# Kernel tuning notes

Hardware: AMD Instinct MI355X
Metric: run time of the kernel (lower is better)

Reference implementation:

```python
import jax, jax.numpy as jnp
import numpy as np


def setup_inputs() -> dict:
    key = jax.random.key(0)
    k1, k2, k3, k4, k5 = jax.random.split(key, 5)
    B, S, D, F, E = 4, 4096, 1024, 2048, 8
    top_k = 2
    num_tokens = B * S
    capacity = max(int(num_tokens / E * 1.25), 4)  # 2560
    scale = 0.02
    return {
        "x": jax.random.normal(k1, (B, S, D), dtype=jnp.float32),
        "gate_w": jax.random.normal(k2, (D, E), dtype=jnp.float32) * scale,
        "w_gate": jax.random.normal(k3, (E, D, F), dtype=jnp.float32) * scale,
        "w_up": jax.random.normal(k4, (E, D, F), dtype=jnp.float32) * scale,
        "w_down": jax.random.normal(k5, (E, F, D), dtype=jnp.float32) * scale,
        "num_experts": E,
        "top_k": top_k,
        "capacity": capacity,
    }


AUX_LOSS_WEIGHT = 0.01


def reference(x, gate_w, w_gate, w_up, w_down, num_experts, top_k, capacity):
    B, S, D = x.shape
    N = B * S
    x_flat = x.reshape(N, D)

    # ---- Router ----
    logits = x_flat @ gate_w                      # [N, E]
    probs = jax.nn.softmax(logits, axis=-1)
    weights, indices = jax.lax.top_k(probs, top_k)  # [N, K]
    weights = weights / jnp.sum(weights, axis=-1, keepdims=True)

    # ---- Capacity-based dispatch ----
    indices_flat = indices.reshape(-1)            # [N*K]
    x_rep = jnp.repeat(x_flat, top_k, axis=0)     # [N*K, D]
    expert_mask = jax.nn.one_hot(indices_flat, num_experts, dtype=jnp.int32)  # [N*K, E]
    token_priority = jnp.cumsum(expert_mask, axis=0) * expert_mask
    token_rank = jnp.sum(token_priority, axis=1)  # [N*K], 1-based rank within expert
    valid = (token_rank > 0) & (token_rank <= capacity)
    gather_idx = indices_flat * capacity + (token_rank - 1)  # [N*K]

    total_slots = num_experts * capacity
    # drop-mode scatter: invalid rows are sent out-of-bounds and dropped
    safe_idx = jnp.where(valid, gather_idx, total_slots)
    dispatched = jnp.zeros((total_slots, D), dtype=x.dtype)
    dispatched = dispatched.at[safe_idx].set(x_rep, mode="drop")
    dispatched = dispatched.reshape(num_experts, capacity, D)  # [E, C, D]

    # ---- Fused experts (grouped BMM, SwiGLU) ----
    gate = jnp.einsum("ecd,edf->ecf", dispatched, w_gate)
    up = jnp.einsum("ecd,edf->ecf", dispatched, w_up)
    hidden = jax.nn.silu(gate) * up
    expert_out = jnp.einsum("ecf,efd->ecd", hidden, w_down)
    expert_out_flat = expert_out.reshape(total_slots, D)

    # ---- Combine (row-aligned gather; dropped tokens contribute zero) ----
    gathered = expert_out_flat[jnp.clip(gather_idx, 0, total_slots - 1)]
    combined = jnp.where(valid[:, None], gathered, jnp.zeros((), dtype=x.dtype))
    combined = combined.reshape(N, top_k, D)
    output = jnp.sum(combined * weights[:, :, None], axis=1)  # [N, D]

    # ---- Aux load-balance loss ----
    mask = jax.nn.one_hot(indices, num_experts, dtype=jnp.float32).sum(axis=1)  # [N, E]
    f = mask.sum(axis=0) / (N * top_k + 1e-9)
    P = probs.mean(axis=0)
    aux_loss = num_experts * jnp.sum(f * P) * AUX_LOSS_WEIGHT

    return output.reshape(B, S, D), aux_loss
```

## Files before the change

### kernel.cpp

```cpp
#include <hip/hip_runtime.h>
#include <stdint.h>

#define N_TOK 16384
#define DIM   1024
#define NEXP  8
#define FF    2048
#define CAP   2560
#define NSLOT (NEXP*CAP)

using f32x4  = __attribute__((ext_vector_type(4))) float;
using bf16x8 = __attribute__((ext_vector_type(8))) short;

__device__ __forceinline__ unsigned short f2bf(float f){
  union { float f; unsigned u; } c; c.f = f;
  unsigned u = c.u + 0x7FFFu + ((c.u >> 16) & 1u);
  return (unsigned short)(u >> 16);
}
__device__ __forceinline__ float bf2f(unsigned short h){
  union { unsigned u; float f; } c; c.u = ((unsigned)h) << 16; return c.f;
}

__device__ __forceinline__ void gld16(const unsigned short* g, unsigned short* l){
  __builtin_amdgcn_global_load_lds((__attribute__((address_space(1))) void*)(void*)g,
                                   (__attribute__((address_space(3))) void*)l,
                                   16, 0, 0);
}

#define HBAR __builtin_amdgcn_s_barrier()
#define LG0  asm volatile("s_waitcnt lgkmcnt(0)" ::: "memory")

__global__ __launch_bounds__(256) void k_router(
    const float* __restrict__ x, const float* __restrict__ gate_w,
    int* __restrict__ topidx, float* __restrict__ topw,
    float* __restrict__ wavepart)
{
  __shared__ float gwT[NEXP][DIM];
  int tid = threadIdx.x;
  for (int i = tid; i < DIM*NEXP; i += 256) gwT[i & 7][i >> 3] = gate_w[i];
  __syncthreads();
  int wave = tid >> 6, lane = tid & 63;
  int t = blockIdx.x * 4 + wave;
  const float* xr = x + (size_t)t * DIM;
  double acc[NEXP];
  #pragma unroll
  for (int e = 0; e < NEXP; e++) acc[e] = 0.0;
  for (int j = 0; j < DIM/64; j++){
    double xv = (double)xr[lane + 64*j];
    #pragma unroll
    for (int e = 0; e < NEXP; e++) acc[e] += xv * (double)gwT[e][lane + 64*j];
  }
  #pragma unroll
  for (int off = 32; off >= 1; off >>= 1){
    #pragma unroll
    for (int e = 0; e < NEXP; e++) acc[e] += __shfl_xor(acc[e], off, 64);
  }
  if (lane == 0){
    double m = acc[0];
    #pragma unroll
    for (int e = 1; e < NEXP; e++) m = fmax(m, acc[e]);
    double p[NEXP], Z = 0.0;
    #pragma unroll
    for (int e = 0; e < NEXP; e++){ p[e] = exp(acc[e] - m); Z += p[e]; }
    double invZ = 1.0 / Z;
    #pragma unroll
    for (int e = 0; e < NEXP; e++) p[e] *= invZ;
    float4* wp = (float4*)(wavepart + (size_t)t*NEXP);
    wp[0] = make_float4((float)p[0], (float)p[1], (float)p[2], (float)p[3]);
    wp[1] = make_float4((float)p[4], (float)p[5], (float)p[6], (float)p[7]);
    int i0 = 0; double p0 = p[0];
    #pragma unroll
    for (int e = 1; e < NEXP; e++) if (p[e] > p0){ p0 = p[e]; i0 = e; }
    int i1 = (i0 == 0) ? 1 : 0; double p1 = p[i1];
    #pragma unroll
    for (int e = 0; e < NEXP; e++) if (e != i0 && p[e] > p1){ p1 = p[e]; i1 = e; }
    double s = p0 + p1;
    topidx[t*2+0] = i0; topidx[t*2+1] = i1;
    topw [t*2+0] = (float)(p0/s); topw[t*2+1] = (float)(p1/s);
  }
}

__global__ __launch_bounds__(1024) void k_scan_tcv(
    const int* __restrict__ topidx, const float* __restrict__ wavepart,
    int* __restrict__ slot_token, int* __restrict__ tok_slots,
    float* __restrict__ aux_out,
    const float* __restrict__ wg, const float* __restrict__ wu, const float* __restrict__ wd,
    unsigned short* __restrict__ B1, unsigned short* __restrict__ wdT,
    const float* __restrict__ x, unsigned short* __restrict__ xb)
{
  __shared__ uint8_t smem[32768];
  const int t = threadIdx.x;
  const int bidx = blockIdx.x;

  if (bidx == 0){
    int (*sc)[NEXP] = (int(*)[NEXP])smem;
    const int base_i = t * 32;
    int ids[32];
    #pragma unroll
    for (int j = 0; j < 32; j++) ids[j] = topidx[base_i + j];
    int b[NEXP];
    #pragma unroll
    for (int e = 0; e < NEXP; e++) b[e] = 0;
    #pragma unroll
    for (int j = 0; j < 32; j++){
      #pragma unroll
      for (int e = 0; e < NEXP; e++) if (ids[j] == e) b[e]++;
    }
    #pragma unroll
    for (int e = 0; e < NEXP; e++) sc[t][e] = b[e];
    __syncthreads();
    for (int off = 1; off < 1024; off <<= 1){
      int tmp[NEXP];
      #pragma unroll
      for (int e = 0; e < NEXP; e++) tmp[e] = (t >= off) ? sc[t-off][e] : 0;
      __syncthreads();
      #pragma unroll
      for (int e = 0; e < NEXP; e++) sc[t][e] += tmp[e];
      __syncthreads();
    }
    int myb[NEXP];
    #pragma unroll
    for (int e = 0; e < NEXP; e++) myb[e] = sc[t][e] - b[e];
    int cnt[NEXP];
    #pragma unroll
    for (int e = 0; e < NEXP; e++) cnt[e] = sc[1023][e];
    #pragma unroll
    for (int j = 0; j < 32; j++){
      int slot = -1;
      #pragma unroll
      for (int e = 0; e < NEXP; e++){
        if (ids[j] == e){
          int r = myb[e]; myb[e] = r + 1;
          if (r < CAP){
            slot = e*CAP + r;
            slot_token[slot] = (base_i + j) >> 1;
          }
        }
      }
      tok_slots[base_i + j] = slot;
    }
    for (int idx = t; idx < NSLOT; idx += 1024){
      int e2 = idx / CAP, r2 = idx - e2*CAP;
      if (r2 >= cnt[e2]) slot_token[idx] = -1;
    }
    __syncthreads();
    float pe[NEXP];
    #pragma unroll
    for (int e = 0; e < NEXP; e++) pe[e] = 0.f;
    for (int i = t; i < N_TOK; i += 1024){
      const float4* pr = (const float4*)(wavepart + (size_t)i*NEXP);
      float4 v0 = pr[0], v1 = pr[1];
      pe[0] += v0.x; pe[1] += v0.y; pe[2] += v0.z; pe[3] += v0.w;
      pe[4] += v1.x; pe[5] += v1.y; pe[6] += v1.z; pe[7] += v1.w;
    }
    #pragma unroll
    for (int off = 32; off >= 1; off >>= 1){
      #pragma unroll
      for (int e = 0; e < NEXP; e++) pe[e] += __shfl_xor(pe[e], off, 64);
    }
    __syncthreads();
    float* scf = (float*)smem;
    const int wv = t >> 6, ln = t & 63;
    if (ln == 0){
      #pragma unroll
      for (int e = 0; e < NEXP; e++) scf[wv*NEXP + e] = pe[e];
    }
    __syncthreads();
    if (t == 0){
      float aux = 0.f;
      #pragma unroll
      for (int e = 0; e < NEXP; e++){
        float P = 0.f;
        for (int w = 0; w < 16; w++) P += scf[w*NEXP + e];
        P /= (float)N_TOK;
        float f = (float)cnt[e] / ((float)(N_TOK*2) + 1e-9f);
        aux += f * P;
      }
      aux_out[0] = (float)NEXP * aux * 0.01f;
    }
  } else if (bidx <= 12288){
    float (*tt)[65] = (float(*)[65])smem;
    const int bid = bidx - 1;
    const int z = bid >> 9, rem = bid & 511;
    const int mode = z >> 3, e = z & 7;
    const float* in; unsigned short* out; int R, C, ct, rt;
    if (mode < 2){
      in  = (mode == 0 ? wg : wu) + (size_t)e * DIM * FF;
      out = B1 + (size_t)e * 2 * FF * DIM;
      R = DIM; C = FF; ct = rem & 31; rt = rem >> 5;
    } else {
      in  = wd + (size_t)e * FF * DIM;
      out = wdT + (size_t)e * DIM * FF;
      R = FF; C = DIM; ct = rem >> 5; rt = rem & 31;
    }
    const int c0 = ct * 64, r0 = rt * 64;
    {
      int row = t >> 4, c4 = t & 15;
      float4 v = *(const float4*)(in + (size_t)(r0 + row)*C + c0 + c4*4);
      tt[c4*4+0][row] = v.x; tt[c4*4+1][row] = v.y;
      tt[c4*4+2][row] = v.z; tt[c4*4+3][row] = v.w;
    }
    __syncthreads();
    {
      int cl = t >> 4;
      int rs = (t & 15) * 4;
      int c  = c0 + cl;
      int orow = (mode == 0) ? ((c>>4)*32 + (c&15))
               : (mode == 1) ? ((c>>4)*32 + 16 + (c&15))
               : c;
      unsigned long long pk = 0;
      #pragma unroll
      for (int j = 0; j < 4; j++) pk |= (unsigned long long)f2bf(tt[cl][rs+j]) << (16*j);
      *(unsigned long long*)(out + (size_t)orow*R + r0 + rs) = pk;
    }
  } else {
    const int gb = bidx - 12289;
    size_t base = ((size_t)gb*1024 + t)*4;
    float4 v = *(const float4*)(x + base);
    unsigned long long pk =
        (unsigned long long)f2bf(v.x)
      | ((unsigned long long)f2bf(v.y) << 16)
      | ((unsigned long long)f2bf(v.z) << 32)
      | ((unsigned long long)f2bf(v.w) << 48);
    *(unsigned long long*)(xb + base) = pk;
  }
}

#define FRD(R_, RR, KS) (*(const bf16x8*)((R_) + (RR)*64 + ((((KS)) ^ l7) << 3)))

#define STGH(TYPE, KT2) {                                                          \
    unsigned short* R_ = lds + ((((KT2)&1)*4 + (TYPE)))*8192;                      \
    if ((TYPE) < 2){                                                               \
      if (EPI == 1){                                                               \
        gld16(Axb + aoff[(TYPE)&1][0] + (KT2)*64, R_ + (wave*8)*64);               \
        gld16(Axb + aoff[(TYPE)&1][1] + (KT2)*64, R_ + (64 + wave*8)*64);          \
      } else {                                                                     \
        gld16(a00 + (size_t)(((TYPE)&1)*128 +  0)*LDG + (KT2)*64, R_ + (wave*8)*64);      \
        gld16(a00 + (size_t)(((TYPE)&1)*128 + 64)*LDG + (KT2)*64, R_ + (64 + wave*8)*64); \
      }                                                                            \
    } else {                                                                       \
      gld16(b00 + (size_t)(((TYPE)&1)*128 +  0)*LDG + (KT2)*64, R_ + (wave*8)*64);        \
      gld16(b00 + (size_t)(((TYPE)&1)*128 + 64)*LDG + (KT2)*64, R_ + (64 + wave*8)*64);   \
    } }

#define MM8(AM, AN, AV, BV)                                                        \
  _Pragma("unroll")                                                                \
  for (int f = 0; f < 4; f++)                                                      \
    _Pragma("unroll")                                                              \
    for (int n = 0; n < 2; n++)                                                    \
      _Pragma("unroll")                                                            \
      for (int kk = 0; kk < 2; kk++)                                               \
        acc[(AM)+f][(AN)+n] = __builtin_amdgcn_mfma_f32_16x16x32_bf16(             \
            AV[f*2+kk], BV[n*2+kk], acc[(AM)+f][(AN)+n], 0, 0, 0);

template<int KDIM, int LDG, int EPI>
__global__ __launch_bounds__(512, 2) void k_gemm8(
    const unsigned short* __restrict__ A,
    const unsigned short* __restrict__ B,
    unsigned short* __restrict__ Out0,
    unsigned short* __restrict__ Out1,
    const int* __restrict__ slot_token)
{
  constexpr int NT    = KDIM / 64;
  constexpr int BROWS = (EPI == 1) ? 2*FF : DIM;
  constexpr int LDO   = (EPI == 1) ? FF : DIM;
  __shared__ unsigned short lds[65536];
  const int id = blockIdx.x;
  const int e  = id & 7;
  int t  = id >> 3;
  int ks = 0;
  if (EPI == 2){ ks = t & 1; t >>= 1; }
  const int mt = t % 10, nt = t / 10;
  const int m0 = mt*256, n0 = nt*256;
  const unsigned short* Ab = A + ((size_t)e*CAP   + m0) * LDG + (size_t)ks*KDIM;
  const unsigned short* Bb = B + ((size_t)e*BROWS + n0) * LDG + (size_t)ks*KDIM;
  const int tid = threadIdx.x, wave = tid >> 6, lane = tid & 63;
  const int wr = wave >> 2, wc = wave & 3;
  const int g = lane >> 4, l15 = lane & 15, l7 = l15 & 7;
  const int srow = lane >> 3, sslot = lane & 7;
  const int kslot_src = sslot ^ srow;

  const unsigned short* Axb = A + (size_t)kslot_src*8;
  unsigned int aoff[2][2];
  const unsigned short* a00 = Ab + (size_t)(wave*8 + srow)*LDG + kslot_src*8;
  const unsigned short* b00 = Bb + (size_t)(wave*8 + srow)*LDG + kslot_src*8;
  if (EPI == 1){
    #pragma unroll
    for (int ah = 0; ah < 2; ah++)
      #pragma unroll
      for (int j = 0; j < 2; j++){
        int row = m0 + ah*128 + j*64 + wave*8 + srow;
        int tk = slot_token[e*CAP + row];
        aoff[ah][j] = (unsigned)((tk < 0 ? 0 : tk) * DIM);
      }
  }

  f32x4 acc[8][4];
  const f32x4 z4 = {0.f,0.f,0.f,0.f};
  #pragma unroll
  for (int i = 0; i < 8; i++)
    #pragma unroll
    for (int n = 0; n < 4; n++) acc[i][n] = z4;

  STGH(0,0); STGH(1,0); STGH(2,0); STGH(3,0);
  STGH(0,1); STGH(1,1); STGH(2,1);
  asm volatile("s_waitcnt vmcnt(6)" ::: "memory");
  HBAR;

  for (int kt = 0; kt < NT; ++kt){
    const int b0 = (kt & 1)*4;
    unsigned short* RA = lds + (b0 + wr)*8192;
    unsigned short* RB = lds + (b0 + 2 + (wc >> 1))*8192;
    const int nb = (wc & 1)*64;
    bf16x8 a0[8], a1[8], bv[4], b2[4];

    #pragma unroll
    for (int f = 0; f < 4; f++)
      #pragma unroll
      for (int kk = 0; kk < 2; kk++)
        a0[f*2+kk] = FRD(RA, f*16 + l15, kk*4 + g);
    #pragma unroll
    for (int n = 0; n < 2; n++)
      #pragma unroll
      for (int kk = 0; kk < 2; kk++)
        bv[n*2+kk] = FRD(RB, nb + n*16 + l15, kk*4 + g);
    if (kt + 1 < NT) STGH(3, kt+1);
    HBAR; LG0;
    __builtin_amdgcn_s_setprio(1);  MM8(0, 0, a0, bv);  __builtin_amdgcn_s_setprio(0);

    #pragma unroll
    for (int f = 0; f < 4; f++)
      #pragma unroll
      for (int kk = 0; kk < 2; kk++)
        a1[f*2+kk] = FRD(RA, 64 + f*16 + l15, kk*4 + g);
    if (kt + 2 < NT) STGH(0, kt+2);
    HBAR; LG0;
    __builtin_amdgcn_s_setprio(1);  MM8(4, 0, a1, bv);  __builtin_amdgcn_s_setprio(0);

    #pragma unroll
    for (int n = 0; n < 2; n++)
      #pragma unroll
      for (int kk = 0; kk < 2; kk++)
        b2[n*2+kk] = FRD(RB, nb + 32 + n*16 + l15, kk*4 + g);
    if (kt + 2 < NT) STGH(1, kt+2);
    HBAR; LG0;
    __builtin_amdgcn_s_setprio(1);  MM8(4, 2, a1, b2);  __builtin_amdgcn_s_setprio(0);

    if (kt + 2 < NT) STGH(2, kt+2);
    __builtin_amdgcn_s_setprio(1);  MM8(0, 2, a0, b2);  __builtin_amdgcn_s_setprio(0);
    if (kt <= NT-3)      { asm volatile("s_waitcnt vmcnt(6)" ::: "memory"); }
    else if (kt == NT-2) { asm volatile("s_waitcnt vmcnt(0)" ::: "memory"); }
    HBAR;
  }

  if (EPI == 1){
    unsigned short* H = Out0 + ((size_t)e*CAP + m0 + wr*128) * (size_t)LDO;
    const int hc0 = (n0 + wc*64) >> 1;
    #pragma unroll
    for (int mf = 0; mf < 8; mf++)
      #pragma unroll
      for (int q = 0; q < 4; q++){
        int r = mf*16 + g*4 + q;
        #pragma unroll
        for (int p = 0; p < 2; p++){
          float gg = acc[mf][2*p][q], uu = acc[mf][2*p+1][q];
          float h = gg / (1.f + __expf(-gg)) * uu;
          H[(size_t)r*LDO + hc0 + p*16 + l15] = f2bf(h);
        }
      }
  } else {
    unsigned short* P = (ks ? Out1 : Out0);
    unsigned short* O = P + ((size_t)e*CAP + m0 + wr*128) * (size_t)LDO + n0 + wc*64;
    #pragma unroll
    for (int mf = 0; mf < 8; mf++)
      #pragma unroll
      for (int q = 0; q < 4; q++){
        int r = mf*16 + g*4 + q;
        #pragma unroll
        for (int n = 0; n < 4; n++)
          O[(size_t)r*LDO + n*16 + l15] = f2bf(acc[mf][n][q]);
      }
  }
}

__global__ __launch_bounds__(256) void k_combine(
    const unsigned short* __restrict__ P0, const unsigned short* __restrict__ P1,
    const int* __restrict__ tok_slots, const float* __restrict__ topw,
    float* __restrict__ out)
{
  const int t = blockIdx.x*2 + (threadIdx.x >> 7);
  const int tid = threadIdx.x & 127;
  const int s0 = tok_slots[t*2+0], s1 = tok_slots[t*2+1];
  const float w0 = topw[t*2+0], w1 = topw[t*2+1];
  float r[8];
  #pragma unroll
  for (int j = 0; j < 8; j++) r[j] = 0.f;
  if (s0 >= 0){
    bf16x8 v0 = *(const bf16x8*)(P0 + (size_t)s0*DIM + tid*8);
    bf16x8 v1 = *(const bf16x8*)(P1 + (size_t)s0*DIM + tid*8);
    #pragma unroll
    for (int j = 0; j < 8; j++)
      r[j] += w0 * (bf2f((unsigned short)v0[j]) + bf2f((unsigned short)v1[j]));
  }
  if (s1 >= 0){
    bf16x8 v0 = *(const bf16x8*)(P0 + (size_t)s1*DIM + tid*8);
    bf16x8 v1 = *(const bf16x8*)(P1 + (size_t)s1*DIM + tid*8);
    #pragma unroll
    for (int j = 0; j < 8; j++)
      r[j] += w1 * (bf2f((unsigned short)v0[j]) + bf2f((unsigned short)v1[j]));
  }
  float4* o = (float4*)(out + (size_t)t*DIM + tid*8);
  o[0] = make_float4(r[0], r[1], r[2], r[3]);
  o[1] = make_float4(r[4], r[5], r[6], r[7]);
}

extern "C" void kernel_launch(void* const* d_in, const int* in_sizes, int n_in,
                              void* d_out, int out_size, void* d_ws, size_t ws_size,
                              hipStream_t stream)
{
  const float* x      = (const float*)d_in[0];
  const float* gate_w = (const float*)d_in[1];
  const float* w_gate = (const float*)d_in[2];
  const float* w_up   = (const float*)d_in[3];
  const float* w_down = (const float*)d_in[4];
  float* out = (float*)d_out;

  uint8_t* ws = (uint8_t*)d_ws;
  int*   topidx       = (int*)ws;               ws += (size_t)N_TOK*2*4;
  float* topw         = (float*)ws;             ws += (size_t)N_TOK*2*4;
  int*   slot_token   = (int*)ws;               ws += (size_t)NSLOT*4;
  int*   tok_slots    = (int*)ws;               ws += (size_t)N_TOK*2*4;
  float* wavepart     = (float*)ws;             ws += (size_t)N_TOK*NEXP*4;
  unsigned short* xb     = (unsigned short*)ws; ws += (size_t)N_TOK*DIM*2;
  unsigned short* P0     = (unsigned short*)ws; ws += (size_t)NSLOT*DIM*2;
  unsigned short* hidden = (unsigned short*)ws; ws += (size_t)NSLOT*FF*2;
  unsigned short* B1     = (unsigned short*)ws; ws += (size_t)NEXP*2*FF*DIM*2;
  unsigned short* wdT    = (unsigned short*)ws; ws += (size_t)NEXP*DIM*FF*2;
  size_t need = (size_t)(ws - (uint8_t*)d_ws);
  if (ws_size < need) return;
  unsigned short* P1 = B1;

  k_router<<<N_TOK/4, 256, 0, stream>>>(x, gate_w, topidx, topw, wavepart);
  k_scan_tcv<<<16385, 1024, 0, stream>>>(topidx, wavepart, slot_token, tok_slots,
                                         out + (size_t)N_TOK*DIM,
                                         w_gate, w_up, w_down, B1, wdT, x, xb);
  k_gemm8<DIM, DIM, 1><<<1280, 512, 0, stream>>>(xb, B1, hidden, nullptr, slot_token);
  k_gemm8<DIM, FF, 2><<<640, 512, 0, stream>>>(hidden, wdT, P0, P1, nullptr);
  k_combine<<<N_TOK/2, 256, 0, stream>>>(P0, P1, tok_slots, topw, out);
}
```

Measured before the change: 423.3 us.

## Split 256x256 GEMM tile across 16 waves instead of 8

After: 560.1 us. 32.3% more time.

```diff
diff --git a/kernel.cpp b/kernel.cpp
--- a/kernel.cpp
+++ b/kernel.cpp
@@ -225,35 +225,14 @@
   }
 }
 
-#define FRD(R_, RR, KS) (*(const bf16x8*)((R_) + (RR)*64 + ((((KS)) ^ l7) << 3)))
-
-#define STGH(TYPE, KT2) {                                                          \
-    unsigned short* R_ = lds + ((((KT2)&1)*4 + (TYPE)))*8192;                      \
-    if ((TYPE) < 2){                                                               \
-      if (EPI == 1){                                                               \
-        gld16(Axb + aoff[(TYPE)&1][0] + (KT2)*64, R_ + (wave*8)*64);               \
-        gld16(Axb + aoff[(TYPE)&1][1] + (KT2)*64, R_ + (64 + wave*8)*64);          \
-      } else {                                                                     \
-        gld16(a00 + (size_t)(((TYPE)&1)*128 +  0)*LDG + (KT2)*64, R_ + (wave*8)*64);      \
-        gld16(a00 + (size_t)(((TYPE)&1)*128 + 64)*LDG + (KT2)*64, R_ + (64 + wave*8)*64); \
-      }                                                                            \
-    } else {                                                                       \
-      gld16(b00 + (size_t)(((TYPE)&1)*128 +  0)*LDG + (KT2)*64, R_ + (wave*8)*64);        \
-      gld16(b00 + (size_t)(((TYPE)&1)*128 + 64)*LDG + (KT2)*64, R_ + (64 + wave*8)*64);   \
-    } }
-
-#define MM8(AM, AN, AV, BV)                                                        \
-  _Pragma("unroll")                                                                \
-  for (int f = 0; f < 4; f++)                                                      \
-    _Pragma("unroll")                                                              \
-    for (int n = 0; n < 2; n++)                                                    \
-      _Pragma("unroll")                                                            \
-      for (int kk = 0; kk < 2; kk++)                                               \
-        acc[(AM)+f][(AN)+n] = __builtin_amdgcn_mfma_f32_16x16x32_bf16(             \
-            AV[f*2+kk], BV[n*2+kk], acc[(AM)+f][(AN)+n], 0, 0, 0);
+#define FRD(R_, RR, KS) (*(const bf16x8*)((R_) + (RR)*64 + (((KS) ^ l7) << 3)))
+#define RGN(KT, TY) (lds + (((KT)&1)*4 + (TY))*8192)
+#define STG_A(KT, H) { if (EPI == 1) gld16(a00 + aoffA[H] + (KT)*64, RGN(KT, H) + wave*512); \
+                       else gld16(a00 + (size_t)(H)*128*LDG + (KT)*64, RGN(KT, H) + wave*512); }
+#define STG_B(KT, H) gld16(b00 + (size_t)(H)*128*LDG + (KT)*64, RGN(KT, (H)+2) + wave*512)
 
 template<int KDIM, int LDG, int EPI>
-__global__ __launch_bounds__(512, 2) void k_gemm8(
+__global__ __launch_bounds__(1024, 4) void k_gemm16(
     const unsigned short* __restrict__ A,
     const unsigned short* __restrict__ B,
     unsigned short* __restrict__ Out0,
@@ -275,88 +254,91 @@
   const unsigned short* Bb = B + ((size_t)e*BROWS + n0) * LDG + (size_t)ks*KDIM;
   const int tid = threadIdx.x, wave = tid >> 6, lane = tid & 63;
   const int wr = wave >> 2, wc = wave & 3;
-  const int g = lane >> 4, l15 = lane & 15, l7 = l15 & 7;
-  const int srow = lane >> 3, sslot = lane & 7;
-  const int kslot_src = sslot ^ srow;
-
-  const unsigned short* Axb = A + (size_t)kslot_src*8;
-  unsigned int aoff[2][2];
-  const unsigned short* a00 = Ab + (size_t)(wave*8 + srow)*LDG + kslot_src*8;
-  const unsigned short* b00 = Bb + (size_t)(wave*8 + srow)*LDG + kslot_src*8;
+  const int g = lane >> 4, l15 = lane & 15, l7 = lane & 7;
+  const int srow = tid >> 3;
+  const int ssl  = (tid & 7) ^ (srow & 7);
+
+  const unsigned short* a00;
+  unsigned aoffA[2] = {0, 0};
   if (EPI == 1){
     #pragma unroll
-    for (int ah = 0; ah < 2; ah++)
-      #pragma unroll
-      for (int j = 0; j < 2; j++){
-        int row = m0 + ah*128 + j*64 + wave*8 + srow;
-        int tk = slot_token[e*CAP + row];
-        aoff[ah][j] = (unsigned)((tk < 0 ? 0 : tk) * DIM);
-      }
-  }
-
-  f32x4 acc[8][4];
+    for (int h = 0; h < 2; h++){
+      int tk = slot_token[e*CAP + m0 + h*128 + srow];
+      aoffA[h] = (unsigned)((tk < 0 ? 0 : tk) * DIM);
+    }
+    a00 = A + ssl*8;
+  } else {
+    a00 = Ab + (size_t)srow*LDG + ssl*8;
+  }
+  const unsigned short* b00 = Bb + (size_t)srow*LDG + ssl*8;
+
+  f32x4 acc[4][4];
   const f32x4 z4 = {0.f,0.f,0.f,0.f};
   #pragma unroll
-  for (int i = 0; i < 8; i++)
+  for (int i = 0; i < 4; i++)
     #pragma unroll
     for (int n = 0; n < 4; n++) acc[i][n] = z4;
 
-  STGH(0,0); STGH(1,0); STGH(2,0); STGH(3,0);
-  STGH(0,1); STGH(1,1); STGH(2,1);
-  asm volatile("s_waitcnt vmcnt(6)" ::: "memory");
+  STG_A(0,0); STG_A(0,1); STG_B(0,0); STG_B(0,1);
+  STG_A(1,0); STG_A(1,1);
+  asm volatile("s_waitcnt vmcnt(2)" ::: "memory");
   HBAR;
 
   for (int kt = 0; kt < NT; ++kt){
-    const int b0 = (kt & 1)*4;
-    unsigned short* RA = lds + (b0 + wr)*8192;
-    unsigned short* RB = lds + (b0 + 2 + (wc >> 1))*8192;
-    const int nb = (wc & 1)*64;
-    bf16x8 a0[8], a1[8], bv[4], b2[4];
+    const unsigned short* RA = RGN(kt, wr >> 1);
+    const unsigned short* RB = RGN(kt, 2 + (wc >> 1));
+    const int ar = (wr & 1)*64, br = (wc & 1)*64;
+    bf16x8 av[8], bl[4], bh[4];
 
     #pragma unroll
     for (int f = 0; f < 4; f++)
       #pragma unroll
       for (int kk = 0; kk < 2; kk++)
-        a0[f*2+kk] = FRD(RA, f*16 + l15, kk*4 + g);
+        av[f*2+kk] = FRD(RA, ar + f*16 + l15, kk*4 + g);
     #pragma unroll
     for (int n = 0; n < 2; n++)
       #pragma unroll
       for (int kk = 0; kk < 2; kk++)
-        bv[n*2+kk] = FRD(RB, nb + n*16 + l15, kk*4 + g);
-    if (kt + 1 < NT) STGH(3, kt+1);
+        bl[n*2+kk] = FRD(RB, br + n*16 + l15, kk*4 + g);
+    if (kt + 1 < NT){ STG_B(kt+1, 0); STG_B(kt+1, 1); }
     HBAR; LG0;
-    __builtin_amdgcn_s_setprio(1);  MM8(0, 0, a0, bv);  __builtin_amdgcn_s_setprio(0);
-
+    __builtin_amdgcn_s_setprio(1);
     #pragma unroll
     for (int f = 0; f < 4; f++)
       #pragma unroll
+      for (int n = 0; n < 2; n++)
+        #pragma unroll
+        for (int kk = 0; kk < 2; kk++)
+          acc[f][n] = __builtin_amdgcn_mfma_f32_16x16x32_bf16(av[f*2+kk], bl[n*2+kk], acc[f][n], 0, 0, 0);
+    __builtin_amdgcn_s_setprio(0);
+
+    #pragma unroll
+    for (int n = 0; n < 2; n++)
+      #pragma unroll
       for (int kk = 0; kk < 2; kk++)
-        a1[f*2+kk] = FRD(RA, 64 + f*16 + l15, kk*4 + g);
-    if (kt + 2 < NT) STGH(0, kt+2);
+        bh[n*2+kk] = FRD(RB, br + (2+n)*16 + l15, kk*4 + g);
+    if (kt + 2 < NT){ STG_A(kt+2, 0); STG_A(kt+2, 1); }
     HBAR; LG0;
-    __builtin_amdgcn_s_setprio(1);  MM8(4, 0, a1, bv);  __builtin_amdgcn_s_setprio(0);
-
-    #pragma unroll
-    for (int n = 0; n < 2; n++)
-      #pragma unroll
-      for (int kk = 0; kk < 2; kk++)
-        b2[n*2+kk] = FRD(RB, nb + 32 + n*16 + l15, kk*4 + g);
-    if (kt + 2 < NT) STGH(1, kt+2);
-    HBAR; LG0;
-    __builtin_amdgcn_s_setprio(1);  MM8(4, 2, a1, b2);  __builtin_amdgcn_s_setprio(0);
-
-    if (kt + 2 < NT) STGH(2, kt+2);
-    __builtin_amdgcn_s_setprio(1);  MM8(0, 2, a0, b2);  __builtin_amdgcn_s_setprio(0);
-    if (kt <= NT-3)      { asm volatile("s_waitcnt vmcnt(6)" ::: "memory"); }
+    __builtin_amdgcn_s_setprio(1);
+    #pragma unroll
+    for (int f = 0; f < 4; f++)
+      #pragma unroll
+      for (int n = 0; n < 2; n++)
+        #pragma unroll
+        for (int kk = 0; kk < 2; kk++)
+          acc[f][2+n] = __builtin_amdgcn_mfma_f32_16x16x32_bf16(av[f*2+kk], bh[n*2+kk], acc[f][2+n], 0, 0, 0);
+    __builtin_amdgcn_s_setprio(0);
+
+    if (kt <= NT-3)      { asm volatile("s_waitcnt vmcnt(2)" ::: "memory"); }
     else if (kt == NT-2) { asm volatile("s_waitcnt vmcnt(0)" ::: "memory"); }
     HBAR;
   }
 
   if (EPI == 1){
-    unsigned short* H = Out0 + ((size_t)e*CAP + m0 + wr*128) * (size_t)LDO;
+    unsigned short* H = Out0 + ((size_t)e*CAP + m0 + wr*64) * (size_t)LDO;
     const int hc0 = (n0 + wc*64) >> 1;
     #pragma unroll
-    for (int mf = 0; mf < 8; mf++)
+    for (int mf = 0; mf < 4; mf++)
       #pragma unroll
       for (int q = 0; q < 4; q++){
         int r = mf*16 + g*4 + q;
@@ -369,9 +351,9 @@
       }
   } else {
     unsigned short* P = (ks ? Out1 : Out0);
-    unsigned short* O = P + ((size_t)e*CAP + m0 + wr*128) * (size_t)LDO + n0 + wc*64;
-    #pragma unroll
-    for (int mf = 0; mf < 8; mf++)
+    unsigned short* O = P + ((size_t)e*CAP + m0 + wr*64) * (size_t)LDO + n0 + wc*64;
+    #pragma unroll
+    for (int mf = 0; mf < 4; mf++)
       #pragma unroll
       for (int q = 0; q < 4; q++){
         int r = mf*16 + g*4 + q;
@@ -443,7 +425,7 @@
   k_scan_tcv<<<16385, 1024, 0, stream>>>(topidx, wavepart, slot_token, tok_slots,
                                          out + (size_t)N_TOK*DIM,
                                          w_gate, w_up, w_down, B1, wdT, x, xb);
-  k_gemm8<DIM, DIM, 1><<<1280, 512, 0, stream>>>(xb, B1, hidden, nullptr, slot_token);
-  k_gemm8<DIM, FF, 2><<<640, 512, 0, stream>>>(hidden, wdT, P0, P1, nullptr);
+  k_gemm16<DIM, DIM, 1><<<1280, 1024, 0, stream>>>(xb, B1, hidden, nullptr, slot_token);
+  k_gemm16<DIM, FF, 2><<<640, 1024, 0, stream>>>(hidden, wdT, P0, P1, nullptr);
   k_combine<<<N_TOK/2, 256, 0, stream>>>(P0, P1, tok_slots, topw, out);
 }
```
